# Kernel tuning notes

Hardware: AMD Instinct MI355X
Metric: run time of the kernel (lower is better)

The kernel has to match this reference:

```python
import jax, jax.numpy as jnp
import numpy as np

N, D = 8192, 1024


def setup_inputs() -> dict:
    key = jax.random.key(0)
    k1, k2, k3, k4 = jax.random.split(key, 4)
    return {
        "first_features": jax.random.normal(k1, (N, D), dtype=jnp.float32),
        "second_features": jax.random.normal(k2, (N, D), dtype=jnp.float32),
        "first_label": jax.random.randint(k3, (N,), 0, N, dtype=jnp.int64),
        "second_label": jax.random.randint(k4, (N,), 0, N, dtype=jnp.int64),
        "logit_scale": jnp.asarray(10.0, dtype=jnp.float32),
        "logit_bias": jnp.asarray(-10.0, dtype=jnp.float32),
    }


def reference(first_features, second_features, first_label, second_label,
              logit_scale, logit_bias):
    # logits: [N, N] = scale * A @ B^T + bias
    logits = logit_scale * jnp.einsum("id,jd->ij", first_features, second_features)
    logits = logits + logit_bias
    # ground truth: +1 where labels match, -1 elsewhere
    labels = jnp.where(first_label[:, None] == second_label[None, :], 1.0, -1.0)
    labels = labels.astype(logits.dtype)
    # loss = sum(-logsigmoid(labels * logits)) / N  (mask_diagonal=False)
    loss = -jnp.sum(jax.nn.log_sigmoid(labels * logits)) / first_features.shape[0]
    return loss
```

## Files before the change

### kernel.cpp

```cpp
#include <hip/hip_runtime.h>
#include <hip/hip_bf16.h>
#include <stdint.h>

#define N_TOK 8192
#define D_K   1024
#define NB    128
#define BKF   128
#define NT    8

typedef __attribute__((ext_vector_type(4))) int   i32x4;
typedef __attribute__((ext_vector_type(8))) int   i32x8;
typedef __attribute__((ext_vector_type(4))) float f32x4;

__global__ void zero_out_kernel(float* out) { out[0] = 0.0f; }

__device__ __forceinline__ unsigned int f32_to_e4m3(float x) {
  uint32_t u = __builtin_bit_cast(uint32_t, x);
  unsigned int s = (u >> 24) & 0x80u;
  float ax = __builtin_fabsf(x);
  if (ax < 0.015625f) {
    int q = (int)rintf(ax * 512.0f);
    return s | (unsigned int)q;
  }
  uint32_t au = u & 0x7FFFFFFFu;
  uint32_t v = au + 0x7FFFFu + ((au >> 20) & 1u);
  int em = (int)(v >> 20) - 960;
  if (em > 0x7E) em = 0x7E;
  return s | (unsigned int)em;
}

__global__ void __launch_bounds__(256)
convert_kernel(const float* __restrict__ a, const float* __restrict__ b,
               unsigned int* __restrict__ oa, unsigned int* __restrict__ ob) {
  const size_t total4 = (size_t)N_TOK * D_K / 4;
  size_t i = (size_t)blockIdx.x * blockDim.x + threadIdx.x;
  size_t stride = (size_t)gridDim.x * blockDim.x;
  for (; i < total4; i += stride) {
    float4 va = ((const float4*)a)[i];
    float4 vb = ((const float4*)b)[i];
    oa[i] = f32_to_e4m3(va.x) | (f32_to_e4m3(va.y) << 8) |
            (f32_to_e4m3(va.z) << 16) | (f32_to_e4m3(va.w) << 24);
    ob[i] = f32_to_e4m3(vb.x) | (f32_to_e4m3(vb.y) << 8) |
            (f32_to_e4m3(vb.z) << 16) | (f32_to_e4m3(vb.w) << 24);
  }
}

__global__ void __launch_bounds__(256, 2)
sigc_kernel(const unsigned char* __restrict__ A8,
            const unsigned char* __restrict__ B8,
            const int* __restrict__ labA, const int* __restrict__ labB,
            const float* __restrict__ scale_p, const float* __restrict__ bias_p,
            float* __restrict__ out) {
  __shared__ unsigned char lds[65536];
  __shared__ int sLabA[NB];
  __shared__ int sLabB[NB];
  __shared__ float sPart[4];

#define LA0 0
#define LA1 16384
#define LB0 32768
#define LB1 49152

  const int tid  = threadIdx.x;
  const int lane = tid & 63;
  const int wid  = tid >> 6;
  const int wr   = wid >> 1;
  const int wc   = wid & 1;
  const int lr   = lane & 15;
  const int kq   = lane >> 4;

  const int bid = (int)blockIdx.x;
  const int xcd = bid & 7;
  const int ii  = bid >> 3;
  const int rr  = (xcd >> 1) * 16 + (ii & 15);
  const int cc  = (xcd & 1) * 32 + (ii >> 4);
  const int bRow = rr * NB;
  const int bCol = cc * NB;

  if (tid < 128)      sLabA[tid] = labA[bRow + tid];
  else                sLabB[tid - 128] = labB[bCol + (tid - 128)];

  const unsigned char* gA[4];
  const unsigned char* gB[4];
#pragma unroll
  for (int ld = 0; ld < 4; ++ld) {
    const int row = ld * 32 + (tid >> 3);
    const int col = ((tid & 7) ^ (row & 7)) << 4;
    gA[ld] = A8 + (size_t)(bRow + row) * D_K + col;
    gB[ld] = B8 + (size_t)(bCol + row) * D_K + col;
  }

  int offA[4], offB[4];
#pragma unroll
  for (int f = 0; f < 4; ++f) {
    const int rA = wr * 64 + f * 16 + lr;
    offA[f] = rA * BKF + (((2 * kq) ^ (rA & 7)) << 4);
    const int rB = wc * 64 + f * 16 + lr;
    offB[f] = rB * BKF + (((2 * kq) ^ (rB & 7)) << 4);
  }

#define STAGE(T, AB, BB) do {                                              \
    _Pragma("unroll") for (int _ld = 0; _ld < 4; ++_ld) {                  \
      __builtin_amdgcn_global_load_lds(                                    \
          (const __attribute__((address_space(1))) void*)(gA[_ld] + (T) * BKF), \
          (__attribute__((address_space(3))) void*)(lds + (AB) + _ld * 4096 + wid * 1024), \
          16, 0, 0);                                                       \
      __builtin_amdgcn_global_load_lds(                                    \
          (const __attribute__((address_space(1))) void*)(gB[_ld] + (T) * BKF), \
          (__attribute__((address_space(3))) void*)(lds + (BB) + _ld * 4096 + wid * 1024), \
          16, 0, 0);                                                       \
    } } while (0)

#define RF(AB, BB, FA, FB) do {                                            \
    _Pragma("unroll") for (int _f = 0; _f < 4; ++_f) {                     \
      ((i32x4*)&FA[_f])[0] = *(const i32x4*)&lds[(AB) + offA[_f]];         \
      ((i32x4*)&FA[_f])[1] = *(const i32x4*)&lds[(AB) + (offA[_f] ^ 16)];  \
      ((i32x4*)&FB[_f])[0] = *(const i32x4*)&lds[(BB) + offB[_f]];         \
      ((i32x4*)&FB[_f])[1] = *(const i32x4*)&lds[(BB) + (offB[_f] ^ 16)];  \
    } } while (0)

#define MMAT(FA, FB) do {                                                  \
    __builtin_amdgcn_s_setprio(1);                                         \
    _Pragma("unroll") for (int _mf = 0; _mf < 4; ++_mf)                    \
    _Pragma("unroll") for (int _nf = 0; _nf < 4; ++_nf)                    \
      acc[_mf][_nf] = __builtin_amdgcn_mfma_scale_f32_16x16x128_f8f6f4(    \
          FA[_mf], FB[_nf], acc[_mf][_nf], 0, 0,                           \
          0, 0x7F7F7F7F, 0, 0x7F7F7F7F);                                   \
    __builtin_amdgcn_s_setprio(0); } while (0)

  f32x4 acc[4][4];
#pragma unroll
  for (int i = 0; i < 4; ++i)
#pragma unroll
    for (int j = 0; j < 4; ++j) acc[i][j] = (f32x4){0.f, 0.f, 0.f, 0.f};

  i32x8 fAe[4], fBe[4], fAo[4], fBo[4];

  STAGE(0, LA0, LB0);
  STAGE(1, LA1, LB1);
  asm volatile("s_waitcnt vmcnt(8)" ::: "memory");
  __syncthreads();
  RF(LA0, LB0, fAe, fBe);

#define ITER(T, FAc, FBc, FAn, FBn, AW, BW, AR, BR) do {                   \
    asm volatile("s_waitcnt lgkmcnt(0)" ::: "memory");                     \
    __builtin_amdgcn_sched_barrier(0);                                     \
    __builtin_amdgcn_s_barrier();                       \
    if ((T) <= 5) {                                                        \
      STAGE((T) + 2, AW, BW);                                              \
      asm volatile("s_waitcnt vmcnt(8)" ::: "memory");                     \
    } else if ((T) == 6) {                                                 \
      asm volatile("s_waitcnt vmcnt(0)" ::: "memory");                     \
    }                                                                      \
    __builtin_amdgcn_sched_barrier(0);                                     \
    __builtin_amdgcn_s_barrier();                  \
    if ((T) <= 6) RF(AR, BR, FAn, FBn);                                    \
    __builtin_amdgcn_sched_barrier(0);                                     \
    MMAT(FAc, FBc);                                                        \
  } while (0)

  ITER(0, fAe, fBe, fAo, fBo, LA0, LB0, LA1, LB1);
  ITER(1, fAo, fBo, fAe, fBe, LA1, LB1, LA0, LB0);
  ITER(2, fAe, fBe, fAo, fBo, LA0, LB0, LA1, LB1);
  ITER(3, fAo, fBo, fAe, fBe, LA1, LB1, LA0, LB0);
  ITER(4, fAe, fBe, fAo, fBo, LA0, LB0, LA1, LB1);
  ITER(5, fAo, fBo, fAe, fBe, LA1, LB1, LA0, LB0);
  ITER(6, fAe, fBe, fAo, fBo, LA0, LB0, LA1, LB1);
  asm volatile("s_waitcnt lgkmcnt(0)" ::: "memory");
  __builtin_amdgcn_sched_barrier(0);
  MMAT(fAo, fBo);

  const float L2E = 1.4426950408889634f;
  const float sl2e = scale_p[0] * L2E;
  const float bl2e = bias_p[0] * L2E;
  float loss = 0.0f;
  const int cBase = lane & 15;
  const int rBase = (lane >> 4) * 4;
#pragma unroll
  for (int mf = 0; mf < 4; ++mf)
#pragma unroll
    for (int nf = 0; nf < 4; ++nf) {
      const int colL = sLabB[wc * 64 + nf * 16 + cBase];
#pragma unroll
      for (int r = 0; r < 4; ++r) {
        const int rowL = sLabA[wr * 64 + mf * 16 + rBase + r];
        const float u0 = fmaf(sl2e, acc[mf][nf][r], bl2e);
        const float u = (rowL == colL) ? -u0 : u0;
        loss += fmaxf(u, 0.0f) + log2f(1.0f + exp2f(-fabsf(u)));
      }
    }

#pragma unroll
  for (int off = 32; off > 0; off >>= 1) loss += __shfl_down(loss, off, 64);
  if (lane == 0) sPart[wid] = loss;
  __syncthreads();
  if (tid == 0) {
    const float s = (sPart[0] + sPart[1]) + (sPart[2] + sPart[3]);
    atomicAdd(out, s * (0.6931471805599453f / (float)N_TOK));
  }
}

extern "C" void kernel_launch(void* const* d_in, const int* in_sizes, int n_in,
                              void* d_out, int out_size, void* d_ws, size_t ws_size,
                              hipStream_t stream) {
  const float* a  = (const float*)d_in[0];
  const float* b  = (const float*)d_in[1];
  const int*   la = (const int*)d_in[2];
  const int*   lb = (const int*)d_in[3];
  const float* sc = (const float*)d_in[4];
  const float* bi = (const float*)d_in[5];
  float* out = (float*)d_out;

  unsigned char* wa = (unsigned char*)d_ws;
  unsigned char* wb = wa + (size_t)N_TOK * D_K;

  zero_out_kernel<<<1, 1, 0, stream>>>(out);
  convert_kernel<<<2048, 256, 0, stream>>>(a, b, (unsigned int*)wa,
                                           (unsigned int*)wb);
  const int grid = (N_TOK / NB) * (N_TOK / NB);
  sigc_kernel<<<grid, 256, 0, stream>>>(wa, wb, la, lb, sc, bi, out);
}
```

Before: 125.4 us.

## Single-buffer LDS and register fragments in FP8 matmul loop to raise occupancy

```diff
diff --git a/kernel.cpp b/kernel.cpp
--- a/kernel.cpp
+++ b/kernel.cpp
@@ -45,21 +45,19 @@
   }
 }
 
-__global__ void __launch_bounds__(256, 2)
+__global__ void __launch_bounds__(256)
 sigc_kernel(const unsigned char* __restrict__ A8,
             const unsigned char* __restrict__ B8,
             const int* __restrict__ labA, const int* __restrict__ labB,
             const float* __restrict__ scale_p, const float* __restrict__ bias_p,
             float* __restrict__ out) {
-  __shared__ unsigned char lds[65536];
+  __shared__ unsigned char lds[32768];
   __shared__ int sLabA[NB];
   __shared__ int sLabB[NB];
   __shared__ float sPart[4];
 
-#define LA0 0
-#define LA1 16384
-#define LB0 32768
-#define LB1 49152
+#define LA 0
+#define LB 16384
 
   const int tid  = threadIdx.x;
   const int lane = tid & 63;
@@ -99,32 +97,32 @@
     offB[f] = rB * BKF + (((2 * kq) ^ (rB & 7)) << 4);
   }
 
-#define STAGE(T, AB, BB) do {                                              \
+#define STAGE(T) do {                                                      \
     _Pragma("unroll") for (int _ld = 0; _ld < 4; ++_ld) {                  \
       __builtin_amdgcn_global_load_lds(                                    \
           (const __attribute__((address_space(1))) void*)(gA[_ld] + (T) * BKF), \
-          (__attribute__((address_space(3))) void*)(lds + (AB) + _ld * 4096 + wid * 1024), \
+          (__attribute__((address_space(3))) void*)(lds + LA + _ld * 4096 + wid * 1024), \
           16, 0, 0);                                                       \
       __builtin_amdgcn_global_load_lds(                                    \
           (const __attribute__((address_space(1))) void*)(gB[_ld] + (T) * BKF), \
-          (__attribute__((address_space(3))) void*)(lds + (BB) + _ld * 4096 + wid * 1024), \
+          (__attribute__((address_space(3))) void*)(lds + LB + _ld * 4096 + wid * 1024), \
           16, 0, 0);                                                       \
     } } while (0)
 
-#define RF(AB, BB, FA, FB) do {                                            \
+#define RF() do {                                                          \
     _Pragma("unroll") for (int _f = 0; _f < 4; ++_f) {                     \
-      ((i32x4*)&FA[_f])[0] = *(const i32x4*)&lds[(AB) + offA[_f]];         \
-      ((i32x4*)&FA[_f])[1] = *(const i32x4*)&lds[(AB) + (offA[_f] ^ 16)];  \
-      ((i32x4*)&FB[_f])[0] = *(const i32x4*)&lds[(BB) + offB[_f]];         \
-      ((i32x4*)&FB[_f])[1] = *(const i32x4*)&lds[(BB) + (offB[_f] ^ 16)];  \
+      ((i32x4*)&fA[_f])[0] = *(const i32x4*)&lds[LA + offA[_f]];           \
+      ((i32x4*)&fA[_f])[1] = *(const i32x4*)&lds[LA + (offA[_f] ^ 16)];    \
+      ((i32x4*)&fB[_f])[0] = *(const i32x4*)&lds[LB + offB[_f]];           \
+      ((i32x4*)&fB[_f])[1] = *(const i32x4*)&lds[LB + (offB[_f] ^ 16)];    \
     } } while (0)
 
-#define MMAT(FA, FB) do {                                                  \
+#define MMAT() do {                                                        \
     __builtin_amdgcn_s_setprio(1);                                         \
     _Pragma("unroll") for (int _mf = 0; _mf < 4; ++_mf)                    \
     _Pragma("unroll") for (int _nf = 0; _nf < 4; ++_nf)                    \
       acc[_mf][_nf] = __builtin_amdgcn_mfma_scale_f32_16x16x128_f8f6f4(    \
-          FA[_mf], FB[_nf], acc[_mf][_nf], 0, 0,                           \
+          fA[_mf], fB[_nf], acc[_mf][_nf], 0, 0,                           \
           0, 0x7F7F7F7F, 0, 0x7F7F7F7F);                                   \
     __builtin_amdgcn_s_setprio(0); } while (0)
 
@@ -134,41 +132,27 @@
 #pragma unroll
     for (int j = 0; j < 4; ++j) acc[i][j] = (f32x4){0.f, 0.f, 0.f, 0.f};
 
-  i32x8 fAe[4], fBe[4], fAo[4], fBo[4];
-
-  STAGE(0, LA0, LB0);
-  STAGE(1, LA1, LB1);
-  asm volatile("s_waitcnt vmcnt(8)" ::: "memory");
+  i32x8 fA[4], fB[4];
+
+  STAGE(0);
+  asm volatile("s_waitcnt vmcnt(0)" ::: "memory");
   __syncthreads();
-  RF(LA0, LB0, fAe, fBe);
-
-#define ITER(T, FAc, FBc, FAn, FBn, AW, BW, AR, BR) do {                   \
-    asm volatile("s_waitcnt lgkmcnt(0)" ::: "memory");                     \
-    __builtin_amdgcn_sched_barrier(0);                                     \
-    __builtin_amdgcn_s_barrier();                       \
-    if ((T) <= 5) {                                                        \
-      STAGE((T) + 2, AW, BW);                                              \
-      asm volatile("s_waitcnt vmcnt(8)" ::: "memory");                     \
-    } else if ((T) == 6) {                                                 \
-      asm volatile("s_waitcnt vmcnt(0)" ::: "memory");                     \
-    }                                                                      \
-    __builtin_amdgcn_sched_barrier(0);                                     \
-    __builtin_amdgcn_s_barrier();                  \
-    if ((T) <= 6) RF(AR, BR, FAn, FBn);                                    \
-    __builtin_amdgcn_sched_barrier(0);                                     \
-    MMAT(FAc, FBc);                                                        \
-  } while (0)
-
-  ITER(0, fAe, fBe, fAo, fBo, LA0, LB0, LA1, LB1);
-  ITER(1, fAo, fBo, fAe, fBe, LA1, LB1, LA0, LB0);
-  ITER(2, fAe, fBe, fAo, fBo, LA0, LB0, LA1, LB1);
-  ITER(3, fAo, fBo, fAe, fBe, LA1, LB1, LA0, LB0);
-  ITER(4, fAe, fBe, fAo, fBo, LA0, LB0, LA1, LB1);
-  ITER(5, fAo, fBo, fAe, fBe, LA1, LB1, LA0, LB0);
-  ITER(6, fAe, fBe, fAo, fBo, LA0, LB0, LA1, LB1);
-  asm volatile("s_waitcnt lgkmcnt(0)" ::: "memory");
-  __builtin_amdgcn_sched_barrier(0);
-  MMAT(fAo, fBo);
+
+#pragma unroll
+  for (int t = 0; t < NT; ++t) {
+    RF();
+    asm volatile("s_waitcnt lgkmcnt(0)" ::: "memory");
+    __builtin_amdgcn_sched_barrier(0);
+    __builtin_amdgcn_s_barrier();
+    if (t < NT - 1) STAGE(t + 1);
+    __builtin_amdgcn_sched_barrier(0);
+    MMAT();
+    if (t < NT - 1) {
+      __builtin_amdgcn_sched_barrier(0);
+      asm volatile("s_waitcnt vmcnt(0)" ::: "memory");
+      __builtin_amdgcn_s_barrier();
+    }
+  }
 
   const float L2E = 1.4426950408889634f;
   const float sl2e = scale_p[0] * L2E;
```

Result: faster. 122.5 us (-2.3%).
